# Kernel tuning notes

Measured on AMD Instinct MI355X. Metric: run time of the kernel, lower is better.

## Reference

```python
import jax, jax.numpy as jnp
import numpy as np

TOPK = 2
NUM_EXPERTS = 8

def setup_inputs() -> dict:
    key = jax.random.key(0)
    kx, kg, k1, k3, k2 = jax.random.split(key, 5)
    B, S, D, F, E = 1, 2048, 1024, 1024, NUM_EXPERTS
    x = jax.random.normal(kx, (B, S, D), dtype=jnp.float32)
    wg = jax.random.normal(kg, (E, D), dtype=jnp.float32) * (1.0 / np.sqrt(D))
    w1 = jax.random.normal(k1, (E, D, F), dtype=jnp.float32) * (1.0 / np.sqrt(D))
    w3 = jax.random.normal(k3, (E, D, F), dtype=jnp.float32) * (1.0 / np.sqrt(D))
    w2 = jax.random.normal(k2, (E, F, D), dtype=jnp.float32) * (1.0 / np.sqrt(F))
    return {"x": x, "wg": wg, "w1": w1, "w3": w3, "w2": w2}

def reference(x, wg, w1, w3, w2):
    # x: [B, S, D] -> tokens [N, D]
    D = x.shape[-1]
    E = wg.shape[0]
    xt = x.reshape(-1, D)
    # Gating: Linear(no bias) + softmax over experts
    logits = xt @ wg.T                      # [N, E]
    gates = jax.nn.softmax(logits, axis=-1)
    # Top-k selection, normalize weights (normalize_expert_weights=True),
    # routed_scaling_factor = 1.0
    weights, idx = jax.lax.top_k(gates, TOPK)      # [N, k]
    weights = weights / weights.sum(axis=-1, keepdims=True)
    # Per-token per-expert combine weight (dispatch+combine equivalent)
    comb = (jax.nn.one_hot(idx, E, dtype=xt.dtype) * weights[..., None]).sum(axis=1)  # [N, E]
    # SwiGLU experts (grouped GEMM equivalent, dense over experts)
    h = jnp.einsum('nd,edf->enf', xt, w1)   # gate proj
    u = jnp.einsum('nd,edf->enf', xt, w3)   # up proj
    a = jax.nn.silu(h) * u                  # [E, N, F]
    out = jnp.einsum('enf,efd,ne->nd', a, w2, comb)
    return out.reshape(x.shape), logits
```

## Files before the change

### kernel.cpp

```cpp
#include <hip/hip_runtime.h>
#include <stdint.h>

typedef unsigned short u16;
typedef __attribute__((ext_vector_type(8))) __bf16 bf16x8;
typedef __attribute__((ext_vector_type(4))) float f32x4;

#define MAXMT 40
#define N_TOK 2048
#define DDIM 1024
#define FDIM 1024

#define DEV static __device__ __forceinline__

DEV float bf2f(u16 u) {
    union { uint32_t i; float f; } v;
    v.i = ((uint32_t)u) << 16;
    return v.f;
}
DEV u16 f2bf(float f) {
    union { float f; uint32_t i; } v;
    v.f = f;
    uint32_t x = v.i;
    return (u16)((x + 0x7fffu + ((x >> 16) & 1u)) >> 16);
}

DEV void async_copy16(const u16* gsrc, u16* ldst) {
    __builtin_amdgcn_global_load_lds(
        (const __attribute__((address_space(1))) void*)(uintptr_t)gsrc,
        (__attribute__((address_space(3))) void*)(uint32_t)(uintptr_t)ldst,
        16, 0, 0);
}

DEV int sniff_fp(const void* p, int tid, int* scnt) {
    if (tid == 0) *scnt = 0;
    __syncthreads();
    u16 u = ((const u16*)p)[tid & 255];
    int e = (u >> 7) & 0xff;
    if (e != 0 && (e < 90 || e > 160)) atomicAdd(scnt, 1);
    __syncthreads();
    return *scnt > 64;
}

__global__ void k_mega(const void* __restrict__ x, const void* __restrict__ wg,
                       const void* __restrict__ w1, const void* __restrict__ w3,
                       const void* __restrict__ w2, u16* __restrict__ wt,
                       u16* __restrict__ xb, void* __restrict__ out_base,
                       int* __restrict__ te, float* __restrict__ tw) {
    __shared__ int scnt;
    __shared__ __align__(16) u16 sT[2][64 * 68];
    int z = blockIdx.z, tid = threadIdx.x;

    if (z >= 2) {
        int zz = z - 2;
        int mat = zz * 2 + (blockIdx.x >> 3);
        int which = mat >> 3, lm = mat & 7;
        const void* src0 = which == 0 ? w1 : (which == 1 ? w3 : w2);
        int fp = sniff_fp(src0, tid, &scnt);
        u16* dst = wt + (size_t)mat * 1048576;
        int rg = tid >> 4, cg = tid & 15;
        int r0 = blockIdx.y * 64, c0 = (blockIdx.x & 7) * 128;
        int rbase = r0 + rg * 4, cbase = c0 + cg * 4;

        u16 vA[4][4], vB[4][4];
        if (fp) {
            const float* sp = (const float*)src0 + (size_t)lm * 1048576;
            float4 fA[4], fB[4];
#pragma unroll
            for (int i = 0; i < 4; i++) fA[i] = *(const float4*)(sp + (size_t)(rbase + i) * 1024 + cbase);
#pragma unroll
            for (int i = 0; i < 4; i++) fB[i] = *(const float4*)(sp + (size_t)(rbase + i) * 1024 + cbase + 64);
#pragma unroll
            for (int i = 0; i < 4; i++) {
                vA[i][0] = f2bf(fA[i].x); vA[i][1] = f2bf(fA[i].y);
                vA[i][2] = f2bf(fA[i].z); vA[i][3] = f2bf(fA[i].w);
                vB[i][0] = f2bf(fB[i].x); vB[i][1] = f2bf(fB[i].y);
                vB[i][2] = f2bf(fB[i].z); vB[i][3] = f2bf(fB[i].w);
            }
        } else {
            const u16* sp = (const u16*)src0 + (size_t)lm * 1048576;
            uint2 uA[4], uB[4];
#pragma unroll
            for (int i = 0; i < 4; i++) uA[i] = *(const uint2*)(sp + (size_t)(rbase + i) * 1024 + cbase);
#pragma unroll
            for (int i = 0; i < 4; i++) uB[i] = *(const uint2*)(sp + (size_t)(rbase + i) * 1024 + cbase + 64);
#pragma unroll
            for (int i = 0; i < 4; i++) { *(uint2*)&vA[i][0] = uA[i]; *(uint2*)&vB[i][0] = uB[i]; }
        }
#pragma unroll
        for (int j = 0; j < 4; j++) {
            uint2 wa, wb;
            wa.x = (uint32_t)vA[0][j] | ((uint32_t)vA[1][j] << 16);
            wa.y = (uint32_t)vA[2][j] | ((uint32_t)vA[3][j] << 16);
            wb.x = (uint32_t)vB[0][j] | ((uint32_t)vB[1][j] << 16);
            wb.y = (uint32_t)vB[2][j] | ((uint32_t)vB[3][j] << 16);
            *(uint2*)&sT[0][(cg * 4 + j) * 68 + rg * 4] = wa;
            *(uint2*)&sT[1][(cg * 4 + j) * 68 + rg * 4] = wb;
        }
        __syncthreads();
        int cc = tid >> 2, seg = tid & 3;
#pragma unroll
        for (int b = 0; b < 2; b++) {
            const u16* spp = &sT[b][cc * 68 + seg * 16];
            uint2 q0 = *(const uint2*)(spp);
            uint2 q1 = *(const uint2*)(spp + 4);
            uint2 q2 = *(const uint2*)(spp + 8);
            uint2 q3 = *(const uint2*)(spp + 12);
            u16* dp = dst + (size_t)(c0 + b * 64 + cc) * 1024 + r0 + seg * 16;
            uint4 o0, o1;
            o0.x = q0.x; o0.y = q0.y; o0.z = q1.x; o0.w = q1.y;
            o1.x = q2.x; o1.y = q2.y; o1.z = q3.x; o1.w = q3.y;
            *(uint4*)dp = o0;
            *(uint4*)(dp + 8) = o1;
        }
    } else {
        int fp = sniff_fp(x, tid, &scnt);
        int gi = z * 256 + blockIdx.y * 16 + blockIdx.x;
        int wave = tid >> 6, lane = tid & 63;
        int n = gi * 4 + wave;
        float acc[8];
#pragma unroll
        for (int e = 0; e < 8; e++) acc[e] = 0.f;
        if (fp) {
            const float* xp = (const float*)x + (size_t)n * DDIM;
            const float* wp = (const float*)wg;
#pragma unroll
            for (int it = 0; it < 4; ++it) {
                int d = it * 256 + lane * 4;
                float4 xv = *(const float4*)(xp + d);
                u16 pk[4] = { f2bf(xv.x), f2bf(xv.y), f2bf(xv.z), f2bf(xv.w) };
                *(uint2*)&xb[(size_t)n * DDIM + d] = *(const uint2*)pk;
#pragma unroll
                for (int e = 0; e < 8; e++) {
                    float4 w4 = *(const float4*)(wp + e * DDIM + d);
                    acc[e] += xv.x * w4.x + xv.y * w4.y + xv.z * w4.z + xv.w * w4.w;
                }
            }
        } else {
            const u16* xp = (const u16*)x + (size_t)n * DDIM;
            const u16* wp = (const u16*)wg;
#pragma unroll
            for (int it = 0; it < 4; ++it) {
                int d = it * 256 + lane * 4;
                uint2 raw = *(const uint2*)(xp + d);
                *(uint2*)&xb[(size_t)n * DDIM + d] = raw;
                const u16* rp = (const u16*)&raw;
                float x0 = bf2f(rp[0]), x1 = bf2f(rp[1]), x2 = bf2f(rp[2]), x3 = bf2f(rp[3]);
#pragma unroll
                for (int e = 0; e < 8; e++) {
                    uint2 wr = *(const uint2*)(wp + e * DDIM + d);
                    const u16* wq = (const u16*)&wr;
                    acc[e] += x0 * bf2f(wq[0]) + x1 * bf2f(wq[1]) + x2 * bf2f(wq[2]) + x3 * bf2f(wq[3]);
                }
            }
        }
#pragma unroll
        for (int e = 0; e < 8; e++) {
            for (int off = 32; off; off >>= 1) acc[e] += __shfl_xor(acc[e], off);
        }
        if (lane < 8) {
            if (fp) ((float*)out_base + (size_t)N_TOK * DDIM)[n * 8 + lane] = acc[lane];
            else    ((u16*)out_base + (size_t)N_TOK * DDIM)[n * 8 + lane] = f2bf(acc[lane]);
        }
        if (lane == 0) {
            int e0 = 0; float b0 = acc[0];
            for (int e = 1; e < 8; e++) if (acc[e] > b0) { b0 = acc[e]; e0 = e; }
            int e1 = -1; float b1 = -1e30f;
            for (int e = 0; e < 8; e++) if (e != e0 && acc[e] > b1) { b1 = acc[e]; e1 = e; }
            float m = fmaxf(b0, b1);
            float x0 = __expf(b0 - m), x1 = __expf(b1 - m);
            float sden = x0 + x1;
            te[n * 2] = e0; te[n * 2 + 1] = e1;
            tw[n * 2] = x0 / sden; tw[n * 2 + 1] = x1 / sden;
        }
    }
}

__global__ void k_sched(const int* __restrict__ te, const float* __restrict__ tw,
                        int* __restrict__ pair_token, float* __restrict__ pair_weight,
                        int* __restrict__ ppos, int* __restrict__ sched) {
    __shared__ int cnt[8], cur[8];
    int t = threadIdx.x;
    if (t < 8) cnt[t] = 0;
    __syncthreads();
    for (int n = t; n < N_TOK; n += 256) {
        atomicAdd(&cnt[te[2 * n]], 1);
        atomicAdd(&cnt[te[2 * n + 1]], 1);
    }
    __syncthreads();
    if (t == 0) {
        int o = 0, mt = 0;
        for (int e = 0; e < 8; e++) {
            cur[e] = o;
            int c = cnt[e];
            for (int m0 = 0; m0 < c; m0 += 128) {
                sched[mt] = e;
                sched[MAXMT + mt] = o + m0;
                sched[2 * MAXMT + mt] = (c - m0 < 128) ? (c - m0) : 128;
                mt++;
            }
            o += c;
        }
        sched[3 * MAXMT] = mt;
        for (int i = mt; i < MAXMT; i++) { sched[i] = 0; sched[MAXMT + i] = 0; sched[2 * MAXMT + i] = 0; }
    }
    __syncthreads();
    for (int n = t; n < N_TOK; n += 256) {
#pragma unroll
        for (int s = 0; s < 2; s++) {
            int e = te[2 * n + s];
            int p = atomicAdd(&cur[e], 1);
            pair_token[p] = n;
            pair_weight[p] = tw[2 * n + s];
            ppos[2 * n + s] = p;
        }
    }
}

__launch_bounds__(256, 2)
__global__ void k_gemm13(const u16* __restrict__ xb, const u16* __restrict__ w1t,
                         const u16* __restrict__ w3t, const int* __restrict__ pair_token,
                         const int* __restrict__ sched, u16* __restrict__ Abuf) {
    __shared__ __align__(16) u16 smem[32768];

    int bn = blockIdx.x;
    int bm = blockIdx.y;
    int total = sched[3 * MAXMT];
    if (bm >= total) return;
    int e = sched[bm];
    int row0 = sched[MAXMT + bm];
    int rowsv = sched[2 * MAXMT + bm];

    int tid = threadIdx.x;
    int wave = tid >> 6, lane = tid & 63;
    int wm = wave & 1, wn = wave >> 1;
    int quad = lane >> 4, l15 = lane & 15;
    int lsub = lane >> 3, slot = lane & 7;

    const u16* gA[4]; int aoff[4];
#pragma unroll
    for (int c = 0; c < 4; c++) {
        int row = c * 32 + wave * 8 + lsub;
        int cr = row < rowsv ? row : 0;
        int tok = pair_token[row0 + cr];
        int gch = slot ^ (row & 7);
        gA[c] = xb + (size_t)tok * DDIM + gch * 8;
        aoff[c] = c * 2048 + wave * 512;
    }
    const u16* gB1[2]; const u16* gB3[2]; int b1off[2], b3off[2];
#pragma unroll
    for (int c = 0; c < 2; c++) {
        int row = c * 32 + wave * 8 + lsub;
        int gch = slot ^ (row & 7);
        int fcol = bn * 64 + row;
        gB1[c] = w1t + ((size_t)e * 1024 + fcol) * 1024 + gch * 8;
        gB3[c] = w3t + ((size_t)e * 1024 + fcol) * 1024 + gch * 8;
        b1off[c] = 8192 + c * 2048 + wave * 512;
        b3off[c] = 12288 + c * 2048 + wave * 512;
    }

    f32x4 acc_h[4][2], acc_u[4][2];
#pragma unroll
    for (int i = 0; i < 4; i++)
#pragma unroll
        for (int j = 0; j < 2; j++) { acc_h[i][j] = (f32x4)0.f; acc_u[i][j] = (f32x4)0.f; }

#pragma unroll
    for (int c = 0; c < 4; c++) async_copy16(gA[c], smem + aoff[c]);
#pragma unroll
    for (int c = 0; c < 2; c++) {
        async_copy16(gB1[c], smem + b1off[c]);
        async_copy16(gB3[c], smem + b3off[c]);
    }

    for (int kt = 0; kt < 16; ++kt) {
        int cur = kt & 1;
        u16* sbuf = smem + cur * 16384;
        __syncthreads();
        if (kt < 15) {
            int k1 = (kt + 1) * 64;
            u16* nbuf = smem + (cur ^ 1) * 16384;
#pragma unroll
            for (int c = 0; c < 4; c++) async_copy16(gA[c] + k1, nbuf + aoff[c]);
#pragma unroll
            for (int c = 0; c < 2; c++) {
                async_copy16(gB1[c] + k1, nbuf + b1off[c]);
                async_copy16(gB3[c] + k1, nbuf + b3off[c]);
            }
        }
        const u16* sA_  = sbuf;
        const u16* sB1_ = sbuf + 8192;
        const u16* sB3_ = sbuf + 12288;
#pragma unroll
        for (int kk = 0; kk < 2; ++kk) {
            bf16x8 a[4], b1[2], b3[2];
#pragma unroll
            for (int i = 0; i < 4; i++) {
                int m = wm * 64 + i * 16 + l15;
                int s = (kk * 4 + quad) ^ (m & 7);
                a[i] = *(const bf16x8*)&sA_[m * 64 + s * 8];
            }
#pragma unroll
            for (int j = 0; j < 2; j++) {
                int nn = wn * 32 + j * 16 + l15;
                int s = (kk * 4 + quad) ^ (nn & 7);
                b1[j] = *(const bf16x8*)&sB1_[nn * 64 + s * 8];
                b3[j] = *(const bf16x8*)&sB3_[nn * 64 + s * 8];
            }
#pragma unroll
            for (int i = 0; i < 4; i++)
#pragma unroll
                for (int j = 0; j < 2; j++) {
                    acc_h[i][j] = __builtin_amdgcn_mfma_f32_16x16x32_bf16(a[i], b1[j], acc_h[i][j], 0, 0, 0);
                    acc_u[i][j] = __builtin_amdgcn_mfma_f32_16x16x32_bf16(a[i], b3[j], acc_u[i][j], 0, 0, 0);
                }
        }
    }
    __syncthreads();
#pragma unroll
    for (int i = 0; i < 4; i++)
#pragma unroll
        for (int j = 0; j < 2; j++)
#pragma unroll
            for (int r = 0; r < 4; r++) {
                int row = wm * 64 + i * 16 + quad * 4 + r;
                int col = wn * 32 + j * 16 + l15;
                float h = acc_h[i][j][r], u = acc_u[i][j][r];
                smem[row * 72 + col] = f2bf(h * u / (1.0f + __expf(-h)));
            }
    __syncthreads();
    int rt = tid >> 1, half = tid & 1;
    if (rt < rowsv) {
        u16* dp = Abuf + (size_t)(row0 + rt) * FDIM + bn * 64 + half * 32;
        const u16* sp = &smem[rt * 72 + half * 32];
#pragma unroll
        for (int q = 0; q < 4; q++)
            *(uint4*)(dp + q * 8) = *(const uint4*)(sp + q * 8);
    }
}

__launch_bounds__(256, 3)
__global__ void k_gemm2(const u16* __restrict__ Abuf, const u16* __restrict__ w2t,
                        const int* __restrict__ sched, u16* __restrict__ Ybuf) {
    __shared__ __align__(16) u16 smem[24576];

    int bn = blockIdx.x;
    int bm = blockIdx.y;
    int total = sched[3 * MAXMT];
    if (bm >= total) return;
    int e = sched[bm];
    int row0 = sched[MAXMT + bm];
    int rowsv = sched[2 * MAXMT + bm];

    int tid = threadIdx.x;
    int wave = tid >> 6, lane = tid & 63;
    int wm = wave & 1, wn = wave >> 1;
    int quad = lane >> 4, l15 = lane & 15;
    int lsub = lane >> 3, slot = lane & 7;

    const u16* gA[4]; int aoff[4];
#pragma unroll
    for (int c = 0; c < 4; c++) {
        int row = c * 32 + wave * 8 + lsub;
        int cr = row < rowsv ? row : 0;
        int gch = slot ^ (row & 7);
        gA[c] = Abuf + (size_t)(row0 + cr) * FDIM + gch * 8;
        aoff[c] = c * 2048 + wave * 512;
    }
    const u16* gB[2]; int boff[2];
#pragma unroll
    for (int c = 0; c < 2; c++) {
        int row = c * 32 + wave * 8 + lsub;
        int gch = slot ^ (row & 7);
        int dcol = bn * 64 + row;
        gB[c] = w2t + ((size_t)e * 1024 + dcol) * 1024 + gch * 8;
        boff[c] = 8192 + c * 2048 + wave * 512;
    }

    f32x4 acc[4][2];
#pragma unroll
    for (int i = 0; i < 4; i++)
#pragma unroll
        for (int j = 0; j < 2; j++) acc[i][j] = (f32x4)0.f;

#pragma unroll
    for (int c = 0; c < 4; c++) async_copy16(gA[c], smem + aoff[c]);
#pragma unroll
    for (int c = 0; c < 2; c++) async_copy16(gB[c], smem + boff[c]);

    for (int kt = 0; kt < 16; ++kt) {
        int cur = kt & 1;
        u16* sbuf = smem + cur * 12288;
        __syncthreads();
        if (kt < 15) {
            int k1 = (kt + 1) * 64;
            u16* nbuf = smem + (cur ^ 1) * 12288;
#pragma unroll
            for (int c = 0; c < 4; c++) async_copy16(gA[c] + k1, nbuf + aoff[c]);
#pragma unroll
            for (int c = 0; c < 2; c++) async_copy16(gB[c] + k1, nbuf + boff[c]);
        }
        const u16* sA_ = sbuf;
        const u16* sB_ = sbuf + 8192;
#pragma unroll
        for (int kk = 0; kk < 2; ++kk) {
            bf16x8 a[4], b[2];
#pragma unroll
            for (int i = 0; i < 4; i++) {
                int m = wm * 64 + i * 16 + l15;
                int s = (kk * 4 + quad) ^ (m & 7);
                a[i] = *(const bf16x8*)&sA_[m * 64 + s * 8];
            }
#pragma unroll
            for (int j = 0; j < 2; j++) {
                int nn = wn * 32 + j * 16 + l15;
                int s = (kk * 4 + quad) ^ (nn & 7);
                b[j] = *(const bf16x8*)&sB_[nn * 64 + s * 8];
            }
#pragma unroll
            for (int i = 0; i < 4; i++)
#pragma unroll
                for (int j = 0; j < 2; j++)
                    acc[i][j] = __builtin_amdgcn_mfma_f32_16x16x32_bf16(a[i], b[j], acc[i][j], 0, 0, 0);
        }
    }
    __syncthreads();
#pragma unroll
    for (int i = 0; i < 4; i++)
#pragma unroll
        for (int j = 0; j < 2; j++)
#pragma unroll
            for (int r = 0; r < 4; r++) {
                int row = wm * 64 + i * 16 + quad * 4 + r;
                int col = wn * 32 + j * 16 + l15;
                smem[row * 72 + col] = f2bf(acc[i][j][r]);
            }
    __syncthreads();
    int rt = tid >> 1, half = tid & 1;
    if (rt < rowsv) {
        u16* dp = Ybuf + (size_t)(row0 + rt) * DDIM + bn * 64 + half * 32;
        const u16* sp = &smem[rt * 72 + half * 32];
#pragma unroll
        for (int q = 0; q < 4; q++)
            *(uint4*)(dp + q * 8) = *(const uint4*)(sp + q * 8);
    }
}

__global__ void k_combine(const u16* __restrict__ Y, const int* __restrict__ ppos,
                          const float* __restrict__ pwt, const void* __restrict__ x,
                          void* __restrict__ out) {
    __shared__ int scnt;
    int n = blockIdx.x, t = threadIdx.x;
    int fp = sniff_fp(x, t, &scnt);
    int p0 = ppos[2 * n], p1 = ppos[2 * n + 1];
    float w0 = pwt[p0], w1 = pwt[p1];
    uint2 a = *(const uint2*)(Y + (size_t)p0 * 1024 + t * 4);
    uint2 b = *(const uint2*)(Y + (size_t)p1 * 1024 + t * 4);
    const u16* ap = (const u16*)&a;
    const u16* bp = (const u16*)&b;
    float r[4];
#pragma unroll
    for (int j = 0; j < 4; j++) r[j] = w0 * bf2f(ap[j]) + w1 * bf2f(bp[j]);
    if (fp) {
        float4 o = { r[0], r[1], r[2], r[3] };
        *(float4*)((float*)out + (size_t)n * 1024 + t * 4) = o;
    } else {
        u16 o[4] = { f2bf(r[0]), f2bf(r[1]), f2bf(r[2]), f2bf(r[3]) };
        *(uint2*)((u16*)out + (size_t)n * 1024 + t * 4) = *(const uint2*)o;
    }
}

extern "C" void kernel_launch(void* const* d_in, const int* in_sizes, int n_in,
                              void* d_out, int out_size, void* d_ws, size_t ws_size,
                              hipStream_t stream) {
    const void* x  = d_in[0];
    const void* wg = d_in[1];
    const void* w1 = d_in[2];
    const void* w3 = d_in[3];
    const void* w2 = d_in[4];

    u16* wt   = (u16*)d_ws;
    u16* w1t  = wt;
    u16* w3t  = wt + (size_t)8 * 1048576;
    u16* w2t  = wt + (size_t)16 * 1048576;
    u16* Abuf = wt + (size_t)24 * 1048576;
    u16* Ybuf = Abuf + (size_t)4096 * 1024;
    u16* xb   = Ybuf + (size_t)4096 * 1024;
    int*   te   = (int*)(xb + (size_t)N_TOK * DDIM);
    float* tw   = (float*)(te + 2 * N_TOK);
    int*   ptok = (int*)(tw + 2 * N_TOK);
    float* pwt  = (float*)(ptok + 2 * N_TOK);
    int*   ppos = (int*)(pwt + 2 * N_TOK);
    int*   sched = ppos + 2 * N_TOK;

    k_mega<<<dim3(16, 16, 14), 256, 0, stream>>>(x, wg, w1, w3, w2, wt, xb, d_out, te, tw);
    k_sched<<<1, 256, 0, stream>>>(te, tw, ptok, pwt, ppos, sched);
    k_gemm13<<<dim3(16, MAXMT), 256, 0, stream>>>(xb, w1t, w3t, ptok, sched, Abuf);
    k_gemm2<<<dim3(16, MAXMT), 256, 0, stream>>>(Abuf, w2t, sched, Ybuf);
    k_combine<<<2048, 256, 0, stream>>>(Ybuf, ppos, pwt, x, d_out);
}
```

Before: 201.3 us.

## Widen GEMM N-tile to 128 and drop double-buffered prefetch

Both expert GEMM kernels now compute 128x128 output tiles instead of 128x64, which halves the grid's N dimension and raises reuse of each loaded A tile. The double-buffered async prefetch is replaced by a single buffer that is loaded and synchronised every k-step, and this cuts shared memory use. The cost is that global loads no longer overlap the MFMA work. Accumulator register pressure roughly doubles (especially in gemm13 with 32 f32x4 per accumulator set), which may cause spills or lower occupancy under the existing launch bounds.

```diff
diff --git a/kernel.cpp b/kernel.cpp
--- a/kernel.cpp
+++ b/kernel.cpp
@@ -220,7 +220,10 @@
 __global__ void k_gemm13(const u16* __restrict__ xb, const u16* __restrict__ w1t,
                          const u16* __restrict__ w3t, const int* __restrict__ pair_token,
                          const int* __restrict__ sched, u16* __restrict__ Abuf) {
-    __shared__ __align__(16) u16 smem[32768];
+    __shared__ __align__(16) u16 smem[24576];
+    u16* sA  = smem;
+    u16* sB1 = smem + 8192;
+    u16* sB3 = smem + 16384;
 
     int bn = blockIdx.x;
     int bm = blockIdx.y;
@@ -237,6 +240,7 @@
     int lsub = lane >> 3, slot = lane & 7;
 
     const u16* gA[4]; int aoff[4];
+    const u16* gB1[4]; const u16* gB3[4]; int boff[4];
 #pragma unroll
     for (int c = 0; c < 4; c++) {
         int row = c * 32 + wave * 8 + lsub;
@@ -245,71 +249,48 @@
         int gch = slot ^ (row & 7);
         gA[c] = xb + (size_t)tok * DDIM + gch * 8;
         aoff[c] = c * 2048 + wave * 512;
-    }
-    const u16* gB1[2]; const u16* gB3[2]; int b1off[2], b3off[2];
-#pragma unroll
-    for (int c = 0; c < 2; c++) {
-        int row = c * 32 + wave * 8 + lsub;
-        int gch = slot ^ (row & 7);
-        int fcol = bn * 64 + row;
+        int fcol = bn * 128 + row;
         gB1[c] = w1t + ((size_t)e * 1024 + fcol) * 1024 + gch * 8;
         gB3[c] = w3t + ((size_t)e * 1024 + fcol) * 1024 + gch * 8;
-        b1off[c] = 8192 + c * 2048 + wave * 512;
-        b3off[c] = 12288 + c * 2048 + wave * 512;
-    }
-
-    f32x4 acc_h[4][2], acc_u[4][2];
+        boff[c] = c * 2048 + wave * 512;
+    }
+
+    f32x4 acc_h[4][4], acc_u[4][4];
 #pragma unroll
     for (int i = 0; i < 4; i++)
 #pragma unroll
-        for (int j = 0; j < 2; j++) { acc_h[i][j] = (f32x4)0.f; acc_u[i][j] = (f32x4)0.f; }
-
-#pragma unroll
-    for (int c = 0; c < 4; c++) async_copy16(gA[c], smem + aoff[c]);
-#pragma unroll
-    for (int c = 0; c < 2; c++) {
-        async_copy16(gB1[c], smem + b1off[c]);
-        async_copy16(gB3[c], smem + b3off[c]);
-    }
+        for (int j = 0; j < 4; j++) { acc_h[i][j] = (f32x4)0.f; acc_u[i][j] = (f32x4)0.f; }
 
     for (int kt = 0; kt < 16; ++kt) {
-        int cur = kt & 1;
-        u16* sbuf = smem + cur * 16384;
+        int k0 = kt * 64;
         __syncthreads();
-        if (kt < 15) {
-            int k1 = (kt + 1) * 64;
-            u16* nbuf = smem + (cur ^ 1) * 16384;
-#pragma unroll
-            for (int c = 0; c < 4; c++) async_copy16(gA[c] + k1, nbuf + aoff[c]);
-#pragma unroll
-            for (int c = 0; c < 2; c++) {
-                async_copy16(gB1[c] + k1, nbuf + b1off[c]);
-                async_copy16(gB3[c] + k1, nbuf + b3off[c]);
-            }
-        }
-        const u16* sA_  = sbuf;
-        const u16* sB1_ = sbuf + 8192;
-        const u16* sB3_ = sbuf + 12288;
+#pragma unroll
+        for (int c = 0; c < 4; c++) {
+            async_copy16(gA[c] + k0, sA + aoff[c]);
+            async_copy16(gB1[c] + k0, sB1 + boff[c]);
+            async_copy16(gB3[c] + k0, sB3 + boff[c]);
+        }
+        __syncthreads();
 #pragma unroll
         for (int kk = 0; kk < 2; ++kk) {
-            bf16x8 a[4], b1[2], b3[2];
+            bf16x8 a[4], b1[4], b3[4];
 #pragma unroll
             for (int i = 0; i < 4; i++) {
                 int m = wm * 64 + i * 16 + l15;
                 int s = (kk * 4 + quad) ^ (m & 7);
-                a[i] = *(const bf16x8*)&sA_[m * 64 + s * 8];
-            }
-#pragma unroll
-            for (int j = 0; j < 2; j++) {
-                int nn = wn * 32 + j * 16 + l15;
+                a[i] = *(const bf16x8*)&sA[m * 64 + s * 8];
+            }
+#pragma unroll
+            for (int j = 0; j < 4; j++) {
+                int nn = wn * 64 + j * 16 + l15;
                 int s = (kk * 4 + quad) ^ (nn & 7);
-                b1[j] = *(const bf16x8*)&sB1_[nn * 64 + s * 8];
-                b3[j] = *(const bf16x8*)&sB3_[nn * 64 + s * 8];
+                b1[j] = *(const bf16x8*)&sB1[nn * 64 + s * 8];
+                b3[j] = *(const bf16x8*)&sB3[nn * 64 + s * 8];
             }
 #pragma unroll
             for (int i = 0; i < 4; i++)
 #pragma unroll
-                for (int j = 0; j < 2; j++) {
+                for (int j = 0; j < 4; j++) {
                     acc_h[i][j] = __builtin_amdgcn_mfma_f32_16x16x32_bf16(a[i], b1[j], acc_h[i][j], 0, 0, 0);
                     acc_u[i][j] = __builtin_amdgcn_mfma_f32_16x16x32_bf16(a[i], b3[j], acc_u[i][j], 0, 0, 0);
                 }
@@ -319,21 +300,21 @@
 #pragma unroll
     for (int i = 0; i < 4; i++)
 #pragma unroll
-        for (int j = 0; j < 2; j++)
+        for (int j = 0; j < 4; j++)
 #pragma unroll
             for (int r = 0; r < 4; r++) {
                 int row = wm * 64 + i * 16 + quad * 4 + r;
-                int col = wn * 32 + j * 16 + l15;
+                int col = wn * 64 + j * 16 + l15;
                 float h = acc_h[i][j][r], u = acc_u[i][j][r];
-                smem[row * 72 + col] = f2bf(h * u / (1.0f + __expf(-h)));
+                smem[row * 136 + col] = f2bf(h * u / (1.0f + __expf(-h)));
             }
     __syncthreads();
     int rt = tid >> 1, half = tid & 1;
     if (rt < rowsv) {
-        u16* dp = Abuf + (size_t)(row0 + rt) * FDIM + bn * 64 + half * 32;
-        const u16* sp = &smem[rt * 72 + half * 32];
-#pragma unroll
-        for (int q = 0; q < 4; q++)
+        u16* dp = Abuf + (size_t)(row0 + rt) * FDIM + bn * 128 + half * 64;
+        const u16* sp = &smem[rt * 136 + half * 64];
+#pragma unroll
+        for (int q = 0; q < 8; q++)
             *(uint4*)(dp + q * 8) = *(const uint4*)(sp + q * 8);
     }
 }
@@ -341,7 +322,9 @@
 __launch_bounds__(256, 3)
 __global__ void k_gemm2(const u16* __restrict__ Abuf, const u16* __restrict__ w2t,
                         const int* __restrict__ sched, u16* __restrict__ Ybuf) {
-    __shared__ __align__(16) u16 smem[24576];
+    __shared__ __align__(16) u16 smem[17408];
+    u16* sA = smem;
+    u16* sB = smem + 8192;
 
     int bn = blockIdx.x;
     int bm = blockIdx.y;
@@ -358,6 +341,7 @@
     int lsub = lane >> 3, slot = lane & 7;
 
     const u16* gA[4]; int aoff[4];
+    const u16* gB[4]; int boff[4];
 #pragma unroll
     for (int c = 0; c < 4; c++) {
         int row = c * 32 + wave * 8 + lsub;
@@ -365,61 +349,45 @@
         int gch = slot ^ (row & 7);
         gA[c] = Abuf + (size_t)(row0 + cr) * FDIM + gch * 8;
         aoff[c] = c * 2048 + wave * 512;
-    }
-    const u16* gB[2]; int boff[2];
-#pragma unroll
-    for (int c = 0; c < 2; c++) {
-        int row = c * 32 + wave * 8 + lsub;
-        int gch = slot ^ (row & 7);
-        int dcol = bn * 64 + row;
+        int dcol = bn * 128 + row;
         gB[c] = w2t + ((size_t)e * 1024 + dcol) * 1024 + gch * 8;
-        boff[c] = 8192 + c * 2048 + wave * 512;
-    }
-
-    f32x4 acc[4][2];
+        boff[c] = c * 2048 + wave * 512;
+    }
+
+    f32x4 acc[4][4];
 #pragma unroll
     for (int i = 0; i < 4; i++)
 #pragma unroll
-        for (int j = 0; j < 2; j++) acc[i][j] = (f32x4)0.f;
-
-#pragma unroll
-    for (int c = 0; c < 4; c++) async_copy16(gA[c], smem + aoff[c]);
-#pragma unroll
-    for (int c = 0; c < 2; c++) async_copy16(gB[c], smem + boff[c]);
+        for (int j = 0; j < 4; j++) acc[i][j] = (f32x4)0.f;
 
     for (int kt = 0; kt < 16; ++kt) {
-        int cur = kt & 1;
-        u16* sbuf = smem + cur * 12288;
+        int k0 = kt * 64;
         __syncthreads();
-        if (kt < 15) {
-            int k1 = (kt + 1) * 64;
-            u16* nbuf = smem + (cur ^ 1) * 12288;
-#pragma unroll
-            for (int c = 0; c < 4; c++) async_copy16(gA[c] + k1, nbuf + aoff[c]);
-#pragma unroll
-            for (int c = 0; c < 2; c++) async_copy16(gB[c] + k1, nbuf + boff[c]);
-        }
-        const u16* sA_ = sbuf;
-        const u16* sB_ = sbuf + 8192;
+#pragma unroll
+        for (int c = 0; c < 4; c++) {
+            async_copy16(gA[c] + k0, sA + aoff[c]);
+            async_copy16(gB[c] + k0, sB + boff[c]);
+        }
+        __syncthreads();
 #pragma unroll
         for (int kk = 0; kk < 2; ++kk) {
-            bf16x8 a[4], b[2];
+            bf16x8 a[4], b[4];
 #pragma unroll
             for (int i = 0; i < 4; i++) {
                 int m = wm * 64 + i * 16 + l15;
                 int s = (kk * 4 + quad) ^ (m & 7);
-                a[i] = *(const bf16x8*)&sA_[m * 64 + s * 8];
-            }
-#pragma unroll
-            for (int j = 0; j < 2; j++) {
-                int nn = wn * 32 + j * 16 + l15;
+                a[i] = *(const bf16x8*)&sA[m * 64 + s * 8];
+            }
+#pragma unroll
+            for (int j = 0; j < 4; j++) {
+                int nn = wn * 64 + j * 16 + l15;
                 int s = (kk * 4 + quad) ^ (nn & 7);
-                b[j] = *(const bf16x8*)&sB_[nn * 64 + s * 8];
+                b[j] = *(const bf16x8*)&sB[nn * 64 + s * 8];
             }
 #pragma unroll
             for (int i = 0; i < 4; i++)
 #pragma unroll
-                for (int j = 0; j < 2; j++)
+                for (int j = 0; j < 4; j++)
                     acc[i][j] = __builtin_amdgcn_mfma_f32_16x16x32_bf16(a[i], b[j], acc[i][j], 0, 0, 0);
         }
     }
@@ -427,20 +395,20 @@
 #pragma unroll
     for (int i = 0; i < 4; i++)
 #pragma unroll
-        for (int j = 0; j < 2; j++)
+        for (int j = 0; j < 4; j++)
 #pragma unroll
             for (int r = 0; r < 4; r++) {
                 int row = wm * 64 + i * 16 + quad * 4 + r;
-                int col = wn * 32 + j * 16 + l15;
-                smem[row * 72 + col] = f2bf(acc[i][j][r]);
+                int col = wn * 64 + j * 16 + l15;
+                smem[row * 136 + col] = f2bf(acc[i][j][r]);
             }
     __syncthreads();
     int rt = tid >> 1, half = tid & 1;
     if (rt < rowsv) {
-        u16* dp = Ybuf + (size_t)(row0 + rt) * DDIM + bn * 64 + half * 32;
-        const u16* sp = &smem[rt * 72 + half * 32];
-#pragma unroll
-        for (int q = 0; q < 4; q++)
+        u16* dp = Ybuf + (size_t)(row0 + rt) * DDIM + bn * 128 + half * 64;
+        const u16* sp = &smem[rt * 136 + half * 64];
+#pragma unroll
+        for (int q = 0; q < 8; q++)
             *(uint4*)(dp + q * 8) = *(const uint4*)(sp + q * 8);
     }
 }
@@ -494,7 +462,7 @@
 
     k_mega<<<dim3(16, 16, 14), 256, 0, stream>>>(x, wg, w1, w3, w2, wt, xb, d_out, te, tw);
     k_sched<<<1, 256, 0, stream>>>(te, tw, ptok, pwt, ppos, sched);
-    k_gemm13<<<dim3(16, MAXMT), 256, 0, stream>>>(xb, w1t, w3t, ptok, sched, Abuf);
-    k_gemm2<<<dim3(16, MAXMT), 256, 0, stream>>>(Abuf, w2t, sched, Ybuf);
+    k_gemm13<<<dim3(8, MAXMT), 256, 0, stream>>>(xb, w1t, w3t, ptok, sched, Abuf);
+    k_gemm2<<<dim3(8, MAXMT), 256, 0, stream>>>(Abuf, w2t, sched, Ybuf);
     k_combine<<<2048, 256, 0, stream>>>(Ybuf, ppos, pwt, x, d_out);
 }
```

After: 208.6 us. 3.6% more time.
